# Performance work log

Hardware: AMD Instinct MI355X
Metric: run time of the kernel (lower is better)

## Reference

```python
import jax, jax.numpy as jnp
import numpy as np

N_NODES = 50000
N_EDGES = 800000
D_FEAT = 64


def setup_inputs() -> dict:
    key = jax.random.key(0)
    k_x, k_e, k_w = jax.random.split(key, 3)
    x = jax.random.normal(k_x, (N_NODES, D_FEAT), dtype=jnp.float32)
    edge_index = jax.random.randint(k_e, (2, N_EDGES), 0, N_NODES, dtype=jnp.int64)
    # message MLP params (phi_Theta): single linear + ReLU
    W = jax.random.normal(k_w, (D_FEAT, D_FEAT), dtype=jnp.float32) / np.sqrt(D_FEAT)
    b = jnp.zeros((D_FEAT,), dtype=jnp.float32)
    return {"x": x, "edge_index": edge_index, "W": W, "b": b}


def reference(x, edge_index, W, b):
    # flow = source_to_target: messages flow from edge_index[0] (j) to edge_index[1] (i)
    src = edge_index[0]  # j: source nodes (gather)
    dst = edge_index[1]  # i: target nodes (scatter index)
    n_nodes = x.shape[0]
    # __collect__: index_select gather of source node features -> x_j [E, D]
    x_j = x[src]
    # message: per-edge MLP  phi(x_j) = relu(x_j W + b)
    msg = jax.nn.relu(jnp.einsum('ed,df->ef', x_j, W) + b)
    # aggregate: scatter-add into target nodes (aggr='add', dim_size = size_i)
    out = jax.ops.segment_sum(msg, dst, num_segments=n_nodes)
    # update: identity
    return out
```

## Files before the change

kernel.cpp:

```cpp
#include <hip/hip_runtime.h>
#include <hip/hip_bf16.h>

#define D 64
#define CAP 32
#define OVF_CAP 16384
#define NSHARD 8
#define TROWS 64


__device__ __forceinline__ float bf2f(unsigned short u) {
    return __uint_as_float((unsigned int)u << 16);
}
__device__ __forceinline__ unsigned short f2bf(float f) {
    unsigned int u = __float_as_uint(f);
    unsigned int r = (u + 0x7fffu + ((u >> 16) & 1u)) >> 16;
    return (unsigned short)r;
}

__global__ __launch_bounds__(256) void node_mlp_lds_kernel(
    const float* __restrict__ x, const float* __restrict__ W,
    const float* __restrict__ b, unsigned short* __restrict__ m,
    int* __restrict__ cnt, int* __restrict__ ovf_cnt, int n_nodes) {
    __shared__ float tile[TROWS][68];
    for (int i = blockIdx.x * blockDim.x + threadIdx.x; i < n_nodes;
         i += gridDim.x * blockDim.x) cnt[i] = 0;
    if (blockIdx.x == 0 && threadIdx.x == 0) *ovf_cnt = 0;

    const int lane = threadIdx.x & 63;
    const int wv = threadIdx.x >> 6;
    float w[D];
    #pragma unroll
    for (int k = 0; k < D; ++k) w[k] = W[k * D + lane];
    const float bias = b[lane];

    for (int t0 = blockIdx.x * TROWS; t0 < n_nodes; t0 += gridDim.x * TROWS) {
        const int nr = min(TROWS, n_nodes - t0);
        {
            const int r = threadIdx.x >> 2, sg = threadIdx.x & 3;
            if (r < nr) {
                const float4* s4 = (const float4*)(x + (size_t)(t0 + r) * D + sg * 16);
                float4 a0 = s4[0], a1 = s4[1], a2 = s4[2], a3 = s4[3];
                float* dl = &tile[r][sg * 16];
                *(float4*)(dl + 0)  = a0;
                *(float4*)(dl + 4)  = a1;
                *(float4*)(dl + 8)  = a2;
                *(float4*)(dl + 12) = a3;
            }
        }
        __syncthreads();
        const int rend = min(wv * 16 + 16, nr);
        for (int rr = wv * 16; rr < rend; rr += 2) {
            const int r0 = rr;
            const int r1 = (rr + 1 < rend) ? rr + 1 : rr;
            float acc0 = bias, acc1 = bias;
            #pragma unroll
            for (int kk = 0; kk < D / 4; ++kk) {
                float4 a = *(const float4*)&tile[r0][4 * kk];
                float4 c = *(const float4*)&tile[r1][4 * kk];
                acc0 = fmaf(a.x, w[4 * kk + 0], acc0);
                acc1 = fmaf(c.x, w[4 * kk + 0], acc1);
                acc0 = fmaf(a.y, w[4 * kk + 1], acc0);
                acc1 = fmaf(c.y, w[4 * kk + 1], acc1);
                acc0 = fmaf(a.z, w[4 * kk + 2], acc0);
                acc1 = fmaf(c.z, w[4 * kk + 2], acc1);
                acc0 = fmaf(a.w, w[4 * kk + 3], acc0);
                acc1 = fmaf(c.w, w[4 * kk + 3], acc1);
            }
            m[(size_t)(t0 + r0) * D + lane] = f2bf(fmaxf(acc0, 0.0f));
            if (r1 > r0)
                m[(size_t)(t0 + r1) * D + lane] = f2bf(fmaxf(acc1, 0.0f));
        }
        __syncthreads();
    }
}

__global__ __launch_bounds__(256) void append_kernel(
    const int* __restrict__ src, const int* __restrict__ dst,
    int* __restrict__ cnt, unsigned short* __restrict__ slots,
    int* __restrict__ ovf_cnt, unsigned int* __restrict__ ovf,
    int n_edges, int blocks_per_shard) {
    const int shard = blockIdx.x & (NSHARD - 1);
    const int p = blockIdx.x >> 3;
    const int chunk = (n_edges + blocks_per_shard - 1) / blocks_per_shard;
    const int beg = p * chunk;
    const int end = min(beg + chunk, n_edges);

    for (int e = beg + (int)threadIdx.x; e < end; e += 256) {
        int d = dst[e];
        if ((d & (NSHARD - 1)) != shard) continue;
        int s = src[e];
        int pos = atomicAdd(&cnt[d], 1);
        if (pos < CAP) {
            slots[(size_t)d * CAP + pos] = (unsigned short)s;
        } else {
            int op = atomicAdd(ovf_cnt, 1);
            if (op < OVF_CAP)
                ovf[op] = ((unsigned int)d << 16) | (unsigned int)s;
        }
    }
}

__global__ __launch_bounds__(256) void gather_kernel(
    const unsigned short* __restrict__ slots, const int* __restrict__ cnt,
    const unsigned short* __restrict__ m,
    const int* __restrict__ ovf_cnt, const unsigned int* __restrict__ ovf,
    float* __restrict__ out, int n_nodes) {
    const int grp = blockIdx.x >> 3;
    const int xcd = blockIdx.x & 7;
    int node = grp * 32 + ((threadIdx.x >> 6) << 3) + xcd;
    if (node >= n_nodes) return;
    node = __builtin_amdgcn_readfirstlane(node);

    const int lane = threadIdx.x & 63;

    const int c = cnt[node];
    const int cc = min(c, CAP);
    const unsigned int* __restrict__ row =
        (const unsigned int*)(slots + (size_t)node * CAP);

    float acc = 0.0f;
    int k = 0;
    for (; k + 16 <= cc; k += 16) {
        unsigned int p[8];
        #pragma unroll
        for (int i = 0; i < 8; ++i) p[i] = row[(k >> 1) + i];
        float v[16];
        #pragma unroll
        for (int i = 0; i < 8; ++i) {
            const unsigned short* ba = m + (size_t)(p[i] & 0xFFFFu) * D;
            const unsigned short* bb = m + (size_t)(p[i] >> 16) * D;
            v[2 * i + 0] = bf2f(ba[lane]);
            v[2 * i + 1] = bf2f(bb[lane]);
        }
        float t0 = ((v[0] + v[1]) + (v[2] + v[3])) + ((v[4] + v[5]) + (v[6] + v[7]));
        float t1 = ((v[8] + v[9]) + (v[10] + v[11])) + ((v[12] + v[13]) + (v[14] + v[15]));
        acc += t0 + t1;
    }
    for (; k + 4 <= cc; k += 4) {
        unsigned int p0 = row[(k >> 1) + 0];
        unsigned int p1 = row[(k >> 1) + 1];
        const unsigned short* b0 = m + (size_t)(p0 & 0xFFFFu) * D;
        const unsigned short* b1 = m + (size_t)(p0 >> 16) * D;
        const unsigned short* b2 = m + (size_t)(p1 & 0xFFFFu) * D;
        const unsigned short* b3 = m + (size_t)(p1 >> 16) * D;
        float v0 = bf2f(b0[lane]);
        float v1 = bf2f(b1[lane]);
        float v2 = bf2f(b2[lane]);
        float v3 = bf2f(b3[lane]);
        acc += (v0 + v1) + (v2 + v3);
    }
    for (; k < cc; ++k) {
        unsigned int p = row[k >> 1];
        unsigned int s = (k & 1) ? (p >> 16) : (p & 0xFFFFu);
        acc += bf2f(m[(size_t)s * D + lane]);
    }
    if (c > CAP) {
        int oc = min(*ovf_cnt, OVF_CAP);
        for (int i = 0; i < oc; ++i) {
            unsigned int e = ovf[i];
            if ((int)(e >> 16) == node)
                acc += bf2f(m[(size_t)(e & 0xFFFFu) * D + lane]);
        }
    }
    out[(size_t)node * D + lane] = acc;
}

__global__ __launch_bounds__(256) void edge_scatter_kernel(
    const int* __restrict__ src, const int* __restrict__ dst,
    const unsigned short* __restrict__ m, float* __restrict__ out, int n_edges) {
    long long t = (long long)blockIdx.x * blockDim.x + threadIdx.x;
    int e = (int)(t >> 4);
    if (e >= n_edges) return;
    int c = (int)(t & 15) << 2;
    int s = src[e];
    int d = dst[e];
    const ushort4 v = *(const ushort4*)(m + (size_t)s * D + c);
    float* o = out + (size_t)d * D + c;
    atomicAdd(o + 0, bf2f(v.x));
    atomicAdd(o + 1, bf2f(v.y));
    atomicAdd(o + 2, bf2f(v.z));
    atomicAdd(o + 3, bf2f(v.w));
}

static inline size_t align_up(size_t v, size_t a) { return (v + a - 1) & ~(a - 1); }

extern "C" void kernel_launch(void* const* d_in, const int* in_sizes, int n_in,
                              void* d_out, int out_size, void* d_ws, size_t ws_size,
                              hipStream_t stream) {
    const float* x = (const float*)d_in[0];
    const int* edge_index = (const int*)d_in[1];
    const float* W = (const float*)d_in[2];
    const float* b = (const float*)d_in[3];
    float* out = (float*)d_out;

    const int n_nodes = in_sizes[0] / D;
    const int n_edges = in_sizes[1] / 2;
    const int* src = edge_index;
    const int* dst = edge_index + n_edges;

    size_t off = 0;
    unsigned short* m = (unsigned short*)((char*)d_ws + off);
    off = align_up(off + (size_t)n_nodes * D * sizeof(unsigned short), 256);
    int* cnt = (int*)((char*)d_ws + off);
    off = align_up(off + (size_t)n_nodes * sizeof(int), 256);
    unsigned short* slots = (unsigned short*)((char*)d_ws + off);
    off = align_up(off + (size_t)n_nodes * CAP * sizeof(unsigned short), 256);
    int* ovf_cnt = (int*)((char*)d_ws + off);
    off = align_up(off + sizeof(int), 256);
    unsigned int* ovf = (unsigned int*)((char*)d_ws + off);
    off = align_up(off + (size_t)OVF_CAP * sizeof(unsigned int), 256);
    const size_t needed = off;

    const int mlp_blocks = (n_nodes + TROWS - 1) / TROWS;
    node_mlp_lds_kernel<<<mlp_blocks, 256, 0, stream>>>(x, W, b, m, cnt, ovf_cnt, n_nodes);

    if (ws_size >= needed && n_nodes <= 65536) {
        const int blocks_per_shard = 320;
        append_kernel<<<blocks_per_shard * NSHARD, 256, 0, stream>>>(
            src, dst, cnt, slots, ovf_cnt, ovf, n_edges, blocks_per_shard);
        const int ngroups = (n_nodes + 31) / 32;
        gather_kernel<<<ngroups * 8, 256, 0, stream>>>(
            slots, cnt, m, ovf_cnt, ovf, out, n_nodes);
    } else {
        hipMemsetAsync(d_out, 0, (size_t)out_size * sizeof(float), stream);
        long long total_threads = (long long)n_edges * 16;
        int scat_blocks = (int)((total_threads + 255) / 256);
        edge_scatter_kernel<<<scat_blocks, 256, 0, stream>>>(src, dst, m, out, n_edges);
    }
}
```

Baseline: 140.2 us.

## Fuse node MLP and edge append into one launch with block-range split

Merges the node MLP kernel and the edge-append bucketing kernel into one launch. The first blocks do the edge appends and the remaining blocks compute the MLP, so the two independent phases overlap. Zeroing of the counters and the overflow counter moves to a single memset over a contiguous span, since the append blocks now need them cleared before they start. This removes one kernel boundary and its tail idle time, at the cost of an extra memset launch and a mixed-role grid whose scheduling may be uneven.

After: 142.5 us. Within noise of the previous version (+1.7%).

```diff
diff --git a/kernel.cpp b/kernel.cpp
--- a/kernel.cpp
+++ b/kernel.cpp
@@ -17,14 +17,41 @@
     return (unsigned short)r;
 }
 
-__global__ __launch_bounds__(256) void node_mlp_lds_kernel(
+__global__ __launch_bounds__(256) void mlp_append_kernel(
     const float* __restrict__ x, const float* __restrict__ W,
     const float* __restrict__ b, unsigned short* __restrict__ m,
-    int* __restrict__ cnt, int* __restrict__ ovf_cnt, int n_nodes) {
+    int n_nodes,
+    const int* __restrict__ src, const int* __restrict__ dst,
+    int* __restrict__ cnt, unsigned short* __restrict__ slots,
+    int* __restrict__ ovf_cnt, unsigned int* __restrict__ ovf,
+    int n_edges, int blocks_per_shard, int append_blocks) {
     __shared__ float tile[TROWS][68];
-    for (int i = blockIdx.x * blockDim.x + threadIdx.x; i < n_nodes;
-         i += gridDim.x * blockDim.x) cnt[i] = 0;
-    if (blockIdx.x == 0 && threadIdx.x == 0) *ovf_cnt = 0;
+
+    if ((int)blockIdx.x < append_blocks) {
+        const int shard = blockIdx.x & (NSHARD - 1);
+        const int p = blockIdx.x >> 3;
+        const int chunk = (n_edges + blocks_per_shard - 1) / blocks_per_shard;
+        const int beg = p * chunk;
+        const int end = min(beg + chunk, n_edges);
+
+        for (int e = beg + (int)threadIdx.x; e < end; e += 256) {
+            int d = dst[e];
+            if ((d & (NSHARD - 1)) != shard) continue;
+            int s = src[e];
+            int pos = atomicAdd(&cnt[d], 1);
+            if (pos < CAP) {
+                slots[(size_t)d * CAP + pos] = (unsigned short)s;
+            } else {
+                int op = atomicAdd(ovf_cnt, 1);
+                if (op < OVF_CAP)
+                    ovf[op] = ((unsigned int)d << 16) | (unsigned int)s;
+            }
+        }
+        return;
+    }
+
+    const int mlpb = (int)blockIdx.x - append_blocks;
+    const int nmlp = (int)gridDim.x - append_blocks;
 
     const int lane = threadIdx.x & 63;
     const int wv = threadIdx.x >> 6;
@@ -33,7 +60,7 @@
     for (int k = 0; k < D; ++k) w[k] = W[k * D + lane];
     const float bias = b[lane];
 
-    for (int t0 = blockIdx.x * TROWS; t0 < n_nodes; t0 += gridDim.x * TROWS) {
+    for (int t0 = mlpb * TROWS; t0 < n_nodes; t0 += nmlp * TROWS) {
         const int nr = min(TROWS, n_nodes - t0);
         {
             const int r = threadIdx.x >> 2, sg = threadIdx.x & 3;
@@ -74,29 +101,60 @@
     }
 }
 
-__global__ __launch_bounds__(256) void append_kernel(
-    const int* __restrict__ src, const int* __restrict__ dst,
-    int* __restrict__ cnt, unsigned short* __restrict__ slots,
-    int* __restrict__ ovf_cnt, unsigned int* __restrict__ ovf,
-    int n_edges, int blocks_per_shard) {
-    const int shard = blockIdx.x & (NSHARD - 1);
-    const int p = blockIdx.x >> 3;
-    const int chunk = (n_edges + blocks_per_shard - 1) / blocks_per_shard;
-    const int beg = p * chunk;
-    const int end = min(beg + chunk, n_edges);
-
-    for (int e = beg + (int)threadIdx.x; e < end; e += 256) {
-        int d = dst[e];
-        if ((d & (NSHARD - 1)) != shard) continue;
-        int s = src[e];
-        int pos = atomicAdd(&cnt[d], 1);
-        if (pos < CAP) {
-            slots[(size_t)d * CAP + pos] = (unsigned short)s;
-        } else {
-            int op = atomicAdd(ovf_cnt, 1);
-            if (op < OVF_CAP)
-                ovf[op] = ((unsigned int)d << 16) | (unsigned int)s;
-        }
+__global__ __launch_bounds__(256) void node_mlp_lds_kernel(
+    const float* __restrict__ x, const float* __restrict__ W,
+    const float* __restrict__ b, unsigned short* __restrict__ m,
+    int* __restrict__ cnt, int* __restrict__ ovf_cnt, int n_nodes) {
+    __shared__ float tile[TROWS][68];
+    for (int i = blockIdx.x * blockDim.x + threadIdx.x; i < n_nodes;
+         i += gridDim.x * blockDim.x) cnt[i] = 0;
+    if (blockIdx.x == 0 && threadIdx.x == 0) *ovf_cnt = 0;
+
+    const int lane = threadIdx.x & 63;
+    const int wv = threadIdx.x >> 6;
+    float w[D];
+    #pragma unroll
+    for (int k = 0; k < D; ++k) w[k] = W[k * D + lane];
+    const float bias = b[lane];
+
+    for (int t0 = blockIdx.x * TROWS; t0 < n_nodes; t0 += gridDim.x * TROWS) {
+        const int nr = min(TROWS, n_nodes - t0);
+        {
+            const int r = threadIdx.x >> 2, sg = threadIdx.x & 3;
+            if (r < nr) {
+                const float4* s4 = (const float4*)(x + (size_t)(t0 + r) * D + sg * 16);
+                float4 a0 = s4[0], a1 = s4[1], a2 = s4[2], a3 = s4[3];
+                float* dl = &tile[r][sg * 16];
+                *(float4*)(dl + 0)  = a0;
+                *(float4*)(dl + 4)  = a1;
+                *(float4*)(dl + 8)  = a2;
+                *(float4*)(dl + 12) = a3;
+            }
+        }
+        __syncthreads();
+        const int rend = min(wv * 16 + 16, nr);
+        for (int rr = wv * 16; rr < rend; rr += 2) {
+            const int r0 = rr;
+            const int r1 = (rr + 1 < rend) ? rr + 1 : rr;
+            float acc0 = bias, acc1 = bias;
+            #pragma unroll
+            for (int kk = 0; kk < D / 4; ++kk) {
+                float4 a = *(const float4*)&tile[r0][4 * kk];
+                float4 c = *(const float4*)&tile[r1][4 * kk];
+                acc0 = fmaf(a.x, w[4 * kk + 0], acc0);
+                acc1 = fmaf(c.x, w[4 * kk + 0], acc1);
+                acc0 = fmaf(a.y, w[4 * kk + 1], acc0);
+                acc1 = fmaf(c.y, w[4 * kk + 1], acc1);
+                acc0 = fmaf(a.z, w[4 * kk + 2], acc0);
+                acc1 = fmaf(c.z, w[4 * kk + 2], acc1);
+                acc0 = fmaf(a.w, w[4 * kk + 3], acc0);
+                acc1 = fmaf(c.w, w[4 * kk + 3], acc1);
+            }
+            m[(size_t)(t0 + r0) * D + lane] = f2bf(fmaxf(acc0, 0.0f));
+            if (r1 > r0)
+                m[(size_t)(t0 + r1) * D + lane] = f2bf(fmaxf(acc1, 0.0f));
+        }
+        __syncthreads();
     }
 }
 
@@ -202,26 +260,29 @@
     unsigned short* m = (unsigned short*)((char*)d_ws + off);
     off = align_up(off + (size_t)n_nodes * D * sizeof(unsigned short), 256);
     int* cnt = (int*)((char*)d_ws + off);
-    off = align_up(off + (size_t)n_nodes * sizeof(int), 256);
+    int* ovf_cnt = cnt + n_nodes;
+    const size_t zero_span = ((size_t)n_nodes + 1) * sizeof(int);
+    off = align_up(off + zero_span, 256);
     unsigned short* slots = (unsigned short*)((char*)d_ws + off);
     off = align_up(off + (size_t)n_nodes * CAP * sizeof(unsigned short), 256);
-    int* ovf_cnt = (int*)((char*)d_ws + off);
-    off = align_up(off + sizeof(int), 256);
     unsigned int* ovf = (unsigned int*)((char*)d_ws + off);
     off = align_up(off + (size_t)OVF_CAP * sizeof(unsigned int), 256);
     const size_t needed = off;
 
-    const int mlp_blocks = (n_nodes + TROWS - 1) / TROWS;
-    node_mlp_lds_kernel<<<mlp_blocks, 256, 0, stream>>>(x, W, b, m, cnt, ovf_cnt, n_nodes);
-
     if (ws_size >= needed && n_nodes <= 65536) {
+        hipMemsetAsync(cnt, 0, zero_span, stream);
         const int blocks_per_shard = 320;
-        append_kernel<<<blocks_per_shard * NSHARD, 256, 0, stream>>>(
-            src, dst, cnt, slots, ovf_cnt, ovf, n_edges, blocks_per_shard);
+        const int append_blocks = blocks_per_shard * NSHARD;
+        const int mlp_blocks = (n_nodes + TROWS - 1) / TROWS;
+        mlp_append_kernel<<<append_blocks + mlp_blocks, 256, 0, stream>>>(
+            x, W, b, m, n_nodes, src, dst, cnt, slots, ovf_cnt, ovf,
+            n_edges, blocks_per_shard, append_blocks);
         const int ngroups = (n_nodes + 31) / 32;
         gather_kernel<<<ngroups * 8, 256, 0, stream>>>(
             slots, cnt, m, ovf_cnt, ovf, out, n_nodes);
     } else {
+        const int mlp_blocks = (n_nodes + TROWS - 1) / TROWS;
+        node_mlp_lds_kernel<<<mlp_blocks, 256, 0, stream>>>(x, W, b, m, cnt, ovf_cnt, n_nodes);
         hipMemsetAsync(d_out, 0, (size_t)out_size * sizeof(float), stream);
         long long total_threads = (long long)n_edges * 16;
         int scat_blocks = (int)((total_threads + 255) / 256);
```
